# Performance work log

Hardware: AMD Instinct MI355X
Metric: run time of the kernel (lower is better)

The kernel has to match this reference:

```python
import jax, jax.numpy as jnp
import numpy as np

N, P, C = 100000, 48, 8
D, H = 64, 4
DH = D // H
FLAG = 7
EPS = 1e-5


def _layer_norm(x, g, b):
    mu = x.mean(-1, keepdims=True)
    var = ((x - mu) ** 2).mean(-1, keepdims=True)
    return (x - mu) * jax.lax.rsqrt(var + EPS) * g + b


def setup_inputs() -> dict:
    key = jax.random.key(0)
    ks = jax.random.split(key, 24)
    w = lambda k, shp: (jax.random.normal(k, shp, dtype=jnp.float32) * 0.05)
    inp = {
        "voxel_features": jax.random.normal(ks[0], (N, D), dtype=jnp.float32),
        "voxels": jax.random.normal(ks[1], (N, P, C), dtype=jnp.float32),
        "pp_w1": w(ks[2], (D, C)), "pp_b1": w(ks[3], (D,)),
        "pp_w2": w(ks[4], (D, D)), "pp_b2": w(ks[5], (D,)),
        "in_proj_w": w(ks[6], (3 * D, D)), "in_proj_b": w(ks[7], (3 * D,)),
        "out_w": w(ks[8], (D, D)), "out_b": w(ks[9], (D,)),
        "ln1_g": jnp.ones((D,), jnp.float32), "ln1_b": jnp.zeros((D,), jnp.float32),
        "ffn_w1": w(ks[10], (2 * D, D)), "ffn_b1": w(ks[11], (2 * D,)),
        "ffn_w2": w(ks[12], (D, 2 * D)), "ffn_b2": w(ks[13], (D,)),
        "ln2_g": jnp.ones((D,), jnp.float32), "ln2_b": jnp.zeros((D,), jnp.float32),
        "op_w1": w(ks[14], (D, D)), "op_b1": w(ks[15], (D,)),
        "op_w2": w(ks[16], (D, D)), "op_b2": w(ks[17], (D,)),
        "num_points": jax.random.randint(ks[18], (N,), 0, P, dtype=jnp.int32),
    }
    return inp


def reference(voxel_features, voxels, pp_w1, pp_b1, pp_w2, pp_b2,
              in_proj_w, in_proj_b, out_w, out_b, ln1_g, ln1_b,
              ffn_w1, ffn_b1, ffn_w2, ffn_b2, ln2_g, ln2_b,
              op_w1, op_b1, op_w2, op_b2, num_points):
    n, p, _ = voxels.shape
    point_mask = jnp.arange(p)[None, :] < num_points[:, None]          # [N,P]
    current_mask = (voxels[:, :, FLAG] > 0.5) & point_mask             # [N,P]
    history_mask = point_mask & ~current_mask                          # [N,P]
    history_present = history_mask.any(axis=1, keepdims=True)          # [N,1]

    point_features = voxels[:, :, :C]

    def masked_mean(vals, mask):
        m = mask.astype(vals.dtype)[..., None]
        counts = jnp.clip(mask.sum(1, keepdims=True), 1, None).astype(vals.dtype)
        return (vals * m).sum(1) / counts                              # [N,C]

    cur_sum = masked_mean(point_features, current_mask)
    his_sum = masked_mean(point_features, history_mask)

    def point_proj(x):
        return jax.nn.relu(x @ pp_w1.T + pp_b1) @ pp_w2.T + pp_b2

    tokens = jnp.stack([voxel_features, point_proj(cur_sum), point_proj(his_sum)], axis=1)  # [N,3,D]

    key_pad = jnp.stack([jnp.zeros((n,), bool),
                         ~current_mask.any(1),
                         ~history_present[:, 0]], axis=1)              # [N,3]

    # multi-head self-attention over 3 tokens
    qkv = tokens @ in_proj_w.T + in_proj_b                             # [N,3,3D]
    q, k, v = jnp.split(qkv, 3, axis=-1)
    q = q.reshape(n, 3, H, DH).transpose(0, 2, 1, 3)                   # [N,H,3,DH]
    k = k.reshape(n, 3, H, DH).transpose(0, 2, 1, 3)
    v = v.reshape(n, 3, H, DH).transpose(0, 2, 1, 3)
    scores = jnp.einsum('nhqd,nhkd->nhqk', q, k) / np.sqrt(DH)
    scores = jnp.where(key_pad[:, None, None, :], -jnp.inf, scores)
    attn = jax.nn.softmax(scores, axis=-1)
    ctx = jnp.einsum('nhqk,nhkd->nhqd', attn, v)                       # [N,H,3,DH]
    ctx = ctx.transpose(0, 2, 1, 3).reshape(n, 3, D)
    attn_out = ctx @ out_w.T + out_b

    tokens = _layer_norm(tokens + attn_out, ln1_g, ln1_b)
    ffn = jax.nn.relu(tokens @ ffn_w1.T + ffn_b1) @ ffn_w2.T + ffn_b2
    tokens = _layer_norm(tokens + ffn, ln2_g, ln2_b)

    refined = jax.nn.relu(tokens[:, 0] @ op_w1.T + op_b1) @ op_w2.T + op_b2
    refined = refined * history_present.astype(refined.dtype)
    return voxel_features + refined
```

## Files before the change

kernel.cpp:

```cpp
#include <hip/hip_runtime.h>


using bf16x8 = __attribute__((ext_vector_type(8))) __bf16;
using f32x4  = __attribute__((ext_vector_type(4))) float;

#define DEV static __device__ __forceinline__

DEV float bf2f(unsigned short u){
  union { unsigned int i; float f; } v; v.i = ((unsigned int)u) << 16; return v.f;
}
DEV unsigned short f2bf(float f){
  union { float f; unsigned int i; } v; v.f = f;
  unsigned int x = v.i;
  x += 0x7FFFu + ((x >> 16) & 1u);
  return (unsigned short)(x >> 16);
}

DEV unsigned short* lp(unsigned short* base, int row, int col){
  int byte = (col << 1) ^ ((row & 7) << 4);
  return (unsigned short*)((char*)base + (row << 7) + byte);
}

DEV bf16x8 ldA(const unsigned short* base, int mt, int kt, int lane){
  int row = mt*16 + (lane & 15);
  int col = kt*32 + ((lane >> 4) << 3);
  return *(const bf16x8*)lp((unsigned short*)base, row, col);
}
DEV bf16x8 ldB(const unsigned short* w, int frag, int lane){
  return *(const bf16x8*)(w + (size_t)frag*512 + (size_t)lane*8);
}
DEV void stC(unsigned short* base, int mt, int nt, f32x4 c, int lane){
  int col  = nt*16 + (lane & 15);
  int row0 = mt*16 + ((lane >> 4) << 2);
  #pragma unroll
  for (int r = 0; r < 4; ++r) *lp(base, row0 + r, col) = f2bf(c[r]);
}
DEV f32x4 MF(bf16x8 a, bf16x8 b, f32x4 c){
  return __builtin_amdgcn_mfma_f32_16x16x32_bf16(a, b, c, 0, 0, 0);
}

DEV void ld16(const unsigned short* base, int row, int col0, float* o){
  uint4 a = *(const uint4*)lp((unsigned short*)base, row, col0);
  uint4 b = *(const uint4*)lp((unsigned short*)base, row, col0 + 8);
  unsigned int w[8] = {a.x, a.y, a.z, a.w, b.x, b.y, b.z, b.w};
  #pragma unroll
  for (int i = 0; i < 8; ++i){
    union { unsigned int u; float f; } lo, hi;
    lo.u = w[i] << 16; hi.u = w[i] & 0xFFFF0000u;
    o[2*i] = lo.f; o[2*i+1] = hi.f;
  }
}
DEV void st16(unsigned short* base, int row, int col0, const float* f){
  unsigned int w[8];
  #pragma unroll
  for (int i = 0; i < 8; ++i)
    w[i] = (unsigned int)f2bf(f[2*i]) | ((unsigned int)f2bf(f[2*i+1]) << 16);
  *(uint4*)lp(base, row, col0)     = make_uint4(w[0], w[1], w[2], w[3]);
  *(uint4*)lp(base, row, col0 + 8) = make_uint4(w[4], w[5], w[6], w[7]);
}

DEV bf16x8 pack8(const float* f){
  union { bf16x8 v; unsigned short u[8]; } r;
  #pragma unroll
  for (int i = 0; i < 8; ++i) r.u[i] = f2bf(f[i]);
  return r.v;
}

DEV void layer_norm16(f32x4 x[4], const float* g, const float* b, int lane){
  float s[4], s2[4];
  #pragma unroll
  for (int r = 0; r < 4; ++r){
    s[r]  = x[0][r] + x[1][r] + x[2][r] + x[3][r];
    s2[r] = x[0][r]*x[0][r] + x[1][r]*x[1][r] + x[2][r]*x[2][r] + x[3][r]*x[3][r];
  }
  #pragma unroll
  for (int o = 1; o <= 8; o <<= 1){
    #pragma unroll
    for (int r = 0; r < 4; ++r){
      s[r]  += __shfl_xor(s[r],  o);
      s2[r] += __shfl_xor(s2[r], o);
    }
  }
  float mu[4], rs[4];
  #pragma unroll
  for (int r = 0; r < 4; ++r){
    mu[r] = s[r] * (1.f/64.f);
    float var = s2[r] * (1.f/64.f) - mu[r]*mu[r];
    rs[r] = rsqrtf(var + 1e-5f);
  }
  const int cl = lane & 15;
  #pragma unroll
  for (int nt = 0; nt < 4; ++nt){
    float gg = g[nt*16 + cl], bb = b[nt*16 + cl];
    #pragma unroll
    for (int r = 0; r < 4; ++r)
      x[nt][r] = (x[nt][r] - mu[r]) * rs[r] * gg + bb;
  }
}

__global__ void tva_pack_weights(const float* __restrict__ pp_w1, const float* __restrict__ pp_w2,
                                 const float* __restrict__ in_proj_w, const float* __restrict__ out_w,
                                 const float* __restrict__ ffn_w1, const float* __restrict__ ffn_w2,
                                 const float* __restrict__ op_w1, const float* __restrict__ op_w2,
                                 unsigned short* __restrict__ ws)
{
  int b = blockIdx.x, lane = threadIdx.x;
  const float* W; int base, ktiles, K;
  if      (b < 4)  { W = pp_w1;     base = 0;  ktiles = 1; K = 8;   }
  else if (b < 12) { W = pp_w2;     base = 4;  ktiles = 2; K = 64;  }
  else if (b < 36) { W = in_proj_w; base = 12; ktiles = 2; K = 64;  }
  else if (b < 44) { W = out_w;     base = 36; ktiles = 2; K = 64;  }
  else if (b < 60) { W = ffn_w1;    base = 44; ktiles = 2; K = 64;  }
  else if (b < 76) { W = ffn_w2;    base = 60; ktiles = 4; K = 128; }
  else if (b < 84) { W = op_w1;     base = 76; ktiles = 2; K = 64;  }
  else             { W = op_w2;     base = 84; ktiles = 2; K = 64;  }
  int local = b - base;
  int nt = local / ktiles, kt = local % ktiles;
  int n  = nt*16 + (lane & 15);
  int k0 = kt*32 + ((lane >> 4) << 3);
  unsigned short* dst = ws + (size_t)b*512 + (size_t)lane*8;
  #pragma unroll
  for (int i = 0; i < 8; ++i){
    int k = k0 + i;
    float v = (k < K) ? W[(size_t)n*K + k] : 0.0f;
    dst[i] = f2bf(v);
  }
}

__global__ __launch_bounds__(256)
void tva_main(const float* __restrict__ vf, const float* __restrict__ vox,
              const int* __restrict__ num_points,
              const float* __restrict__ pp_b1, const float* __restrict__ pp_b2,
              const float* __restrict__ ipb,  const float* __restrict__ outb,
              const float* __restrict__ ln1g, const float* __restrict__ ln1b,
              const float* __restrict__ f1b,  const float* __restrict__ f2bv,
              const float* __restrict__ ln2g, const float* __restrict__ ln2b,
              const float* __restrict__ o1b,  const float* __restrict__ o2b,
              const unsigned short* __restrict__ wfrag,
              float* __restrict__ out, int nvox)
{
  __shared__ unsigned short smem[4 * 64 * 64];
  const int tid  = threadIdx.x;
  const int wv   = tid >> 6;
  const int lane = tid & 63;
  unsigned short* X = smem + wv * (64*64);
  unsigned short* Q = X + 48*64;

  const int v0 = (blockIdx.x * 4 + wv) * 16;
  if (v0 >= nvox) return;
  const int cl = lane & 15;
  const int r0 = (lane >> 4) << 2;

  const int vi = lane >> 2, pq = lane & 3;
  const int np = num_points[v0 + vi];
  float cs[8] = {0,0,0,0,0,0,0,0}, hs[8] = {0,0,0,0,0,0,0,0};
  float cc = 0.f, hc = 0.f;
  const float4* vp = (const float4*)(vox + (size_t)(v0 + vi) * 384);
  #pragma unroll
  for (int k = 0; k < 12; ++k){
    int p = pq + (k << 2);
    float4 a = vp[p*2], b = vp[p*2 + 1];
    float pm = (p < np) ? 1.f : 0.f;
    float cm = (b.w > 0.5f) ? pm : 0.f;
    float hm = pm - cm;
    cc += cm; hc += hm;
    cs[0] += a.x*cm; cs[1] += a.y*cm; cs[2] += a.z*cm; cs[3] += a.w*cm;
    cs[4] += b.x*cm; cs[5] += b.y*cm; cs[6] += b.z*cm; cs[7] += b.w*cm;
    hs[0] += a.x*hm; hs[1] += a.y*hm; hs[2] += a.z*hm; hs[3] += a.w*hm;
    hs[4] += b.x*hm; hs[5] += b.y*hm; hs[6] += b.z*hm; hs[7] += b.w*hm;
  }
  #pragma unroll
  for (int o = 1; o <= 2; o <<= 1){
    cc += __shfl_xor(cc, o); hc += __shfl_xor(hc, o);
    #pragma unroll
    for (int j = 0; j < 8; ++j){
      cs[j] += __shfl_xor(cs[j], o);
      hs[j] += __shfl_xor(hs[j], o);
    }
  }
  const float icc = 1.f / fmaxf(cc, 1.f);
  const float ihc = 1.f / fmaxf(hc, 1.f);
  const unsigned int myfw = (cc > 0.f ? 1u : 0u) | (hc > 0.f ? 2u : 0u);

  bf16x8 ac, ah;
  {
    const int src = cl * 4;
    float cf[8], hf[8];
    #pragma unroll
    for (int i = 0; i < 8; ++i){
      cf[i] = __shfl(cs[i]*icc, src);
      hf[i] = __shfl(hs[i]*ihc, src);
    }
    union { bf16x8 v; unsigned short u[8]; } rc, rh;
    #pragma unroll
    for (int i = 0; i < 8; ++i){
      rc.u[i] = (lane < 16) ? f2bf(cf[i]) : (unsigned short)0;
      rh.u[i] = (lane < 16) ? f2bf(hf[i]) : (unsigned short)0;
    }
    ac = rc.v; ah = rh.v;
  }

  #pragma unroll
  for (int nt = 0; nt < 4; ++nt){
    float bb = pp_b1[nt*16 + cl];
    f32x4 c0 = {bb, bb, bb, bb}, c1 = {bb, bb, bb, bb};
    bf16x8 B = ldB(wfrag, nt, lane);
    c0 = MF(ac, B, c0);
    c1 = MF(ah, B, c1);
    #pragma unroll
    for (int r = 0; r < 4; ++r){ c0[r] = fmaxf(c0[r], 0.f); c1[r] = fmaxf(c1[r], 0.f); }
    stC(X, 0, nt, c0, lane);
    stC(X, 1, nt, c1, lane);
  }
  {
    bf16x8 hfr[2][2];
    #pragma unroll
    for (int m = 0; m < 2; ++m)
      #pragma unroll
      for (int kt = 0; kt < 2; ++kt) hfr[m][kt] = ldA(X, m, kt, lane);
    #pragma unroll
    for (int m = 0; m < 2; ++m){
      #pragma unroll
      for (int nt = 0; nt < 4; ++nt){
        float bb = pp_b2[nt*16 + cl];
        f32x4 c = {bb, bb, bb, bb};
        c = MF(hfr[m][0], ldB(wfrag, 4 + nt*2 + 0, lane), c);
        c = MF(hfr[m][1], ldB(wfrag, 4 + nt*2 + 1, lane), c);
        stC(X, m, nt, c, lane);
      }
    }
  }

  bf16x8 at[3][2];
  {
    const float* s = vf + (size_t)(v0 + cl) * 64 + ((lane >> 4) << 3);
    #pragma unroll
    for (int kt = 0; kt < 2; ++kt){
      float4 x0 = *(const float4*)(s + kt*32);
      float4 x1 = *(const float4*)(s + kt*32 + 4);
      float f[8] = {x0.x, x0.y, x0.z, x0.w, x1.x, x1.y, x1.z, x1.w};
      at[0][kt] = pack8(f);
    }
    #pragma unroll
    for (int kt = 0; kt < 2; ++kt){
      at[1][kt] = ldA(X, 0, kt, lane);
      at[2][kt] = ldA(X, 1, kt, lane);
    }
  }
  #pragma unroll
  for (int nt = 0; nt < 4; ++nt){
    float bb = ipb[nt*16 + cl];
    f32x4 c = {bb, bb, bb, bb};
    c = MF(at[0][0], ldB(wfrag, 12 + nt*2 + 0, lane), c);
    c = MF(at[0][1], ldB(wfrag, 12 + nt*2 + 1, lane), c);
    #pragma unroll
    for (int r = 0; r < 4; ++r) c[r] *= 0.25f;
    stC(Q, 0, nt, c, lane);
  }
  #pragma unroll
  for (int m = 0; m < 3; ++m){
    #pragma unroll
    for (int nt = 0; nt < 4; ++nt){
      int ntg = 4 + nt;
      float bb = ipb[64 + nt*16 + cl];
      f32x4 c = {bb, bb, bb, bb};
      c = MF(at[m][0], ldB(wfrag, 12 + ntg*2 + 0, lane), c);
      c = MF(at[m][1], ldB(wfrag, 12 + ntg*2 + 1, lane), c);
      stC(X, m, nt, c, lane);
    }
  }

  const int av = cl, hh2 = lane >> 4;
  float p0, p1, p2;
  {
    unsigned int fw = (unsigned int)__shfl((int)myfw, av*4);
    bool caZ = (fw & 1u) != 0, hpZ = (fw & 2u) != 0;
    float q[16]; ld16(Q, av, hh2*16, q);
    float sc[3];
    #pragma unroll
    for (int m = 0; m < 3; ++m){
      float kv[16]; ld16(X, m*16 + av, hh2*16, kv);
      float d = 0.f;
      #pragma unroll
      for (int j = 0; j < 16; ++j) d += q[j]*kv[j];
      sc[m] = d;
    }
    float mx = sc[0];
    mx = caZ ? fmaxf(mx, sc[1]) : mx;
    mx = hpZ ? fmaxf(mx, sc[2]) : mx;
    p0 = __expf(sc[0] - mx);
    p1 = caZ ? __expf(sc[1] - mx) : 0.f;
    p2 = hpZ ? __expf(sc[2] - mx) : 0.f;
    float inv = 1.f / (p0 + p1 + p2);
    p0 *= inv; p1 *= inv; p2 *= inv;
  }

  #pragma unroll
  for (int m = 0; m < 3; ++m){
    #pragma unroll
    for (int nt = 0; nt < 4; ++nt){
      int ntg = 8 + nt;
      float bb = ipb[128 + nt*16 + cl];
      f32x4 c = {bb, bb, bb, bb};
      c = MF(at[m][0], ldB(wfrag, 12 + ntg*2 + 0, lane), c);
      c = MF(at[m][1], ldB(wfrag, 12 + ntg*2 + 1, lane), c);
      stC(X, m, nt, c, lane);
    }
  }

  {
    float ctx[16];
    float vv[16];
    ld16(X, av, hh2*16, vv);
    #pragma unroll
    for (int j = 0; j < 16; ++j) ctx[j] = p0*vv[j];
    ld16(X, 16 + av, hh2*16, vv);
    #pragma unroll
    for (int j = 0; j < 16; ++j) ctx[j] += p1*vv[j];
    ld16(X, 32 + av, hh2*16, vv);
    #pragma unroll
    for (int j = 0; j < 16; ++j) ctx[j] += p2*vv[j];
    st16(Q, av, hh2*16, ctx);
  }

  f32x4 res1[4];
  {
    bf16x8 a0 = ldA(Q, 0, 0, lane), a1 = ldA(Q, 0, 1, lane);
    float rv[16];
    #pragma unroll
    for (int nt = 0; nt < 4; ++nt)
      #pragma unroll
      for (int r = 0; r < 4; ++r)
        rv[nt*4 + r] = vf[(size_t)(v0 + r0 + r)*64 + nt*16 + cl];
    #pragma unroll
    for (int nt = 0; nt < 4; ++nt){
      float bb = outb[nt*16 + cl];
      f32x4 c = {bb, bb, bb, bb};
      c = MF(a0, ldB(wfrag, 36 + nt*2 + 0, lane), c);
      c = MF(a1, ldB(wfrag, 36 + nt*2 + 1, lane), c);
      #pragma unroll
      for (int r = 0; r < 4; ++r) c[r] += rv[nt*4 + r];
      res1[nt] = c;
    }
    layer_norm16(res1, ln1g, ln1b, lane);
    #pragma unroll
    for (int nt = 0; nt < 4; ++nt) stC(Q, 0, nt, res1[nt], lane);
  }

  f32x4 tk2[4];
  {
    bf16x8 a0 = ldA(Q, 0, 0, lane), a1 = ldA(Q, 0, 1, lane);
    #pragma unroll
    for (int nt = 0; nt < 4; ++nt){
      float bb = f2bv[nt*16 + cl];
      tk2[nt] = (f32x4){bb, bb, bb, bb};
    }
    #pragma unroll
    for (int nt = 0; nt < 4; ++nt){
      float bb = f1b[nt*16 + cl];
      f32x4 c = {bb, bb, bb, bb};
      c = MF(a0, ldB(wfrag, 44 + nt*2 + 0, lane), c);
      c = MF(a1, ldB(wfrag, 44 + nt*2 + 1, lane), c);
      #pragma unroll
      for (int r = 0; r < 4; ++r) c[r] = fmaxf(c[r], 0.f);
      stC(X, 0, nt, c, lane);
    }
    {
      bf16x8 h0 = ldA(X, 0, 0, lane), h1 = ldA(X, 0, 1, lane);
      #pragma unroll
      for (int nt = 0; nt < 4; ++nt){
        tk2[nt] = MF(h0, ldB(wfrag, 60 + nt*4 + 0, lane), tk2[nt]);
        tk2[nt] = MF(h1, ldB(wfrag, 60 + nt*4 + 1, lane), tk2[nt]);
      }
    }
    #pragma unroll
    for (int nt = 4; nt < 8; ++nt){
      float bb = f1b[nt*16 + cl];
      f32x4 c = {bb, bb, bb, bb};
      c = MF(a0, ldB(wfrag, 44 + nt*2 + 0, lane), c);
      c = MF(a1, ldB(wfrag, 44 + nt*2 + 1, lane), c);
      #pragma unroll
      for (int r = 0; r < 4; ++r) c[r] = fmaxf(c[r], 0.f);
      stC(X, 0, nt - 4, c, lane);
    }
    {
      bf16x8 h0 = ldA(X, 0, 0, lane), h1 = ldA(X, 0, 1, lane);
      #pragma unroll
      for (int nt = 0; nt < 4; ++nt){
        tk2[nt] = MF(h0, ldB(wfrag, 60 + nt*4 + 2, lane), tk2[nt]);
        tk2[nt] = MF(h1, ldB(wfrag, 60 + nt*4 + 3, lane), tk2[nt]);
      }
    }
    #pragma unroll
    for (int nt = 0; nt < 4; ++nt)
      #pragma unroll
      for (int r = 0; r < 4; ++r) tk2[nt][r] += res1[nt][r];
    layer_norm16(tk2, ln2g, ln2b, lane);
    #pragma unroll
    for (int nt = 0; nt < 4; ++nt) stC(Q, 0, nt, tk2[nt], lane);
  }

  {
    bf16x8 a0 = ldA(Q, 0, 0, lane), a1 = ldA(Q, 0, 1, lane);
    #pragma unroll
    for (int nt = 0; nt < 4; ++nt){
      float bb = o1b[nt*16 + cl];
      f32x4 c = {bb, bb, bb, bb};
      c = MF(a0, ldB(wfrag, 76 + nt*2 + 0, lane), c);
      c = MF(a1, ldB(wfrag, 76 + nt*2 + 1, lane), c);
      #pragma unroll
      for (int r = 0; r < 4; ++r) c[r] = fmaxf(c[r], 0.f);
      stC(X, 0, nt, c, lane);
    }
    bf16x8 b0 = ldA(X, 0, 0, lane), b1 = ldA(X, 0, 1, lane);
    #pragma unroll
    for (int nt = 0; nt < 4; ++nt){
      float bb = o2b[nt*16 + cl];
      f32x4 c = {bb, bb, bb, bb};
      c = MF(b0, ldB(wfrag, 84 + nt*2 + 0, lane), c);
      c = MF(b1, ldB(wfrag, 84 + nt*2 + 1, lane), c);
      #pragma unroll
      for (int r = 0; r < 4; ++r){
        int row = r0 + r;
        unsigned int fw2 = (unsigned int)__shfl((int)myfw, row*4);
        float keep = (fw2 & 2u) ? 1.f : 0.f;
        size_t idx = (size_t)(v0 + row)*64 + nt*16 + cl;
        out[idx] = vf[idx] + keep * c[r];
      }
    }
  }
}

extern "C" void kernel_launch(void* const* d_in, const int* in_sizes, int n_in,
                              void* d_out, int out_size, void* d_ws, size_t ws_size,
                              hipStream_t stream)
{
  (void)n_in; (void)out_size; (void)ws_size;
  const float* vf    = (const float*)d_in[0];
  const float* vox   = (const float*)d_in[1];
  const float* pp_w1 = (const float*)d_in[2];
  const float* pp_b1 = (const float*)d_in[3];
  const float* pp_w2 = (const float*)d_in[4];
  const float* pp_b2 = (const float*)d_in[5];
  const float* ipw   = (const float*)d_in[6];
  const float* ipb   = (const float*)d_in[7];
  const float* outw  = (const float*)d_in[8];
  const float* outb  = (const float*)d_in[9];
  const float* ln1g  = (const float*)d_in[10];
  const float* ln1b  = (const float*)d_in[11];
  const float* f1w   = (const float*)d_in[12];
  const float* f1b   = (const float*)d_in[13];
  const float* f2w   = (const float*)d_in[14];
  const float* f2b   = (const float*)d_in[15];
  const float* ln2g  = (const float*)d_in[16];
  const float* ln2b  = (const float*)d_in[17];
  const float* o1w   = (const float*)d_in[18];
  const float* o1b   = (const float*)d_in[19];
  const float* o2w   = (const float*)d_in[20];
  const float* o2b   = (const float*)d_in[21];
  const int*   npts  = (const int*)d_in[22];
  unsigned short* wfrag = (unsigned short*)d_ws;
  float* out = (float*)d_out;

  const int nvox = in_sizes[0] / 64;
  const int ngrp = nvox / 16;
  const int nblk = (ngrp + 3) / 4;
  tva_pack_weights<<<92, 64, 0, stream>>>(pp_w1, pp_w2, ipw, outw, f1w, f2w, o1w, o2w, wfrag);
  tva_main<<<nblk, 256, 0, stream>>>(vf, vox, npts, pp_b1, pp_b2, ipb, outb,
                                     ln1g, ln1b, f1b, f2b, ln2g, ln2b, o1b, o2b,
                                     wfrag, out, nvox);
}
```

Baseline: 75.09 us.

## Swap MFMA operands so accumulators hold voxel-major rows, vectorising I/O and layernorm

Result: slower. 84.57 us (+12.6%).

```diff
diff --git a/kernel.cpp b/kernel.cpp
--- a/kernel.cpp
+++ b/kernel.cpp
@@ -6,9 +6,6 @@
 
 #define DEV static __device__ __forceinline__
 
-DEV float bf2f(unsigned short u){
-  union { unsigned int i; float f; } v; v.i = ((unsigned int)u) << 16; return v.f;
-}
 DEV unsigned short f2bf(float f){
   union { float f; unsigned int i; } v; v.f = f;
   unsigned int x = v.i;
@@ -21,22 +18,27 @@
   return (unsigned short*)((char*)base + (row << 7) + byte);
 }
 
-DEV bf16x8 ldA(const unsigned short* base, int mt, int kt, int lane){
-  int row = mt*16 + (lane & 15);
+DEV bf16x8 ldA(const unsigned short* base, int tt, int kt, int lane){
+  int row = tt*16 + (lane & 15);
   int col = kt*32 + ((lane >> 4) << 3);
   return *(const bf16x8*)lp((unsigned short*)base, row, col);
 }
-DEV bf16x8 ldB(const unsigned short* w, int frag, int lane){
+DEV bf16x8 ldW(const unsigned short* w, int frag, int lane){
   return *(const bf16x8*)(w + (size_t)frag*512 + (size_t)lane*8);
 }
-DEV void stC(unsigned short* base, int mt, int nt, f32x4 c, int lane){
-  int col  = nt*16 + (lane & 15);
-  int row0 = mt*16 + ((lane >> 4) << 2);
-  #pragma unroll
-  for (int r = 0; r < 4; ++r) *lp(base, row0 + r, col) = f2bf(c[r]);
+DEV void stC(unsigned short* base, int tt, int mt, f32x4 c, int lane){
+  int trow = tt*16 + (lane & 15);
+  int col0 = mt*16 + ((lane >> 4) << 2);
+  unsigned int lo = (unsigned int)f2bf(c[0]) | ((unsigned int)f2bf(c[1]) << 16);
+  unsigned int hi = (unsigned int)f2bf(c[2]) | ((unsigned int)f2bf(c[3]) << 16);
+  *(uint2*)lp(base, trow, col0) = make_uint2(lo, hi);
 }
 DEV f32x4 MF(bf16x8 a, bf16x8 b, f32x4 c){
   return __builtin_amdgcn_mfma_f32_16x16x32_bf16(a, b, c, 0, 0, 0);
+}
+DEV f32x4 bias4(const float* p){
+  float4 b = *(const float4*)p;
+  return (f32x4){b.x, b.y, b.z, b.w};
 }
 
 DEV void ld16(const unsigned short* base, int row, int col0, float* o){
@@ -66,35 +68,25 @@
   return r.v;
 }
 
-DEV void layer_norm16(f32x4 x[4], const float* g, const float* b, int lane){
-  float s[4], s2[4];
-  #pragma unroll
-  for (int r = 0; r < 4; ++r){
-    s[r]  = x[0][r] + x[1][r] + x[2][r] + x[3][r];
-    s2[r] = x[0][r]*x[0][r] + x[1][r]*x[1][r] + x[2][r]*x[2][r] + x[3][r]*x[3][r];
-  }
-  #pragma unroll
-  for (int o = 1; o <= 8; o <<= 1){
-    #pragma unroll
-    for (int r = 0; r < 4; ++r){
-      s[r]  += __shfl_xor(s[r],  o);
-      s2[r] += __shfl_xor(s2[r], o);
-    }
-  }
-  float mu[4], rs[4];
-  #pragma unroll
-  for (int r = 0; r < 4; ++r){
-    mu[r] = s[r] * (1.f/64.f);
-    float var = s2[r] * (1.f/64.f) - mu[r]*mu[r];
-    rs[r] = rsqrtf(var + 1e-5f);
-  }
-  const int cl = lane & 15;
+DEV void layer_norm_sw(f32x4 x[4], const float* g, const float* b, int lane){
+  float s = 0.f, s2 = 0.f;
+  #pragma unroll
+  for (int nt = 0; nt < 4; ++nt)
+    #pragma unroll
+    for (int r = 0; r < 4; ++r){ s += x[nt][r]; s2 += x[nt][r]*x[nt][r]; }
+  s  += __shfl_xor(s, 16);  s2 += __shfl_xor(s2, 16);
+  s  += __shfl_xor(s, 32);  s2 += __shfl_xor(s2, 32);
+  float mu = s * (1.f/64.f);
+  float rs = rsqrtf(s2 * (1.f/64.f) - mu*mu + 1e-5f);
+  const int r0 = (lane >> 4) << 2;
   #pragma unroll
   for (int nt = 0; nt < 4; ++nt){
-    float gg = g[nt*16 + cl], bb = b[nt*16 + cl];
-    #pragma unroll
-    for (int r = 0; r < 4; ++r)
-      x[nt][r] = (x[nt][r] - mu[r]) * rs[r] * gg + bb;
+    float4 gg = *(const float4*)&g[nt*16 + r0];
+    float4 bb = *(const float4*)&b[nt*16 + r0];
+    x[nt][0] = (x[nt][0] - mu) * rs * gg.x + bb.x;
+    x[nt][1] = (x[nt][1] - mu) * rs * gg.y + bb.y;
+    x[nt][2] = (x[nt][2] - mu) * rs * gg.z + bb.z;
+    x[nt][3] = (x[nt][3] - mu) * rs * gg.w + bb.w;
   }
 }
 
@@ -202,11 +194,10 @@
 
   #pragma unroll
   for (int nt = 0; nt < 4; ++nt){
-    float bb = pp_b1[nt*16 + cl];
-    f32x4 c0 = {bb, bb, bb, bb}, c1 = {bb, bb, bb, bb};
-    bf16x8 B = ldB(wfrag, nt, lane);
-    c0 = MF(ac, B, c0);
-    c1 = MF(ah, B, c1);
+    f32x4 binit = bias4(&pp_b1[nt*16 + r0]);
+    bf16x8 W = ldW(wfrag, nt, lane);
+    f32x4 c0 = MF(W, ac, binit);
+    f32x4 c1 = MF(W, ah, binit);
     #pragma unroll
     for (int r = 0; r < 4; ++r){ c0[r] = fmaxf(c0[r], 0.f); c1[r] = fmaxf(c1[r], 0.f); }
     stC(X, 0, nt, c0, lane);
@@ -219,13 +210,14 @@
       #pragma unroll
       for (int kt = 0; kt < 2; ++kt) hfr[m][kt] = ldA(X, m, kt, lane);
     #pragma unroll
-    for (int m = 0; m < 2; ++m){
-      #pragma unroll
-      for (int nt = 0; nt < 4; ++nt){
-        float bb = pp_b2[nt*16 + cl];
-        f32x4 c = {bb, bb, bb, bb};
-        c = MF(hfr[m][0], ldB(wfrag, 4 + nt*2 + 0, lane), c);
-        c = MF(hfr[m][1], ldB(wfrag, 4 + nt*2 + 1, lane), c);
+    for (int nt = 0; nt < 4; ++nt){
+      f32x4 binit = bias4(&pp_b2[nt*16 + r0]);
+      bf16x8 W0 = ldW(wfrag, 4 + nt*2 + 0, lane);
+      bf16x8 W1 = ldW(wfrag, 4 + nt*2 + 1, lane);
+      #pragma unroll
+      for (int m = 0; m < 2; ++m){
+        f32x4 c = MF(W0, hfr[m][0], binit);
+        c = MF(W1, hfr[m][1], c);
         stC(X, m, nt, c, lane);
       }
     }
@@ -249,23 +241,23 @@
   }
   #pragma unroll
   for (int nt = 0; nt < 4; ++nt){
-    float bb = ipb[nt*16 + cl];
-    f32x4 c = {bb, bb, bb, bb};
-    c = MF(at[0][0], ldB(wfrag, 12 + nt*2 + 0, lane), c);
-    c = MF(at[0][1], ldB(wfrag, 12 + nt*2 + 1, lane), c);
+    f32x4 c = bias4(&ipb[nt*16 + r0]);
+    c = MF(ldW(wfrag, 12 + nt*2 + 0, lane), at[0][0], c);
+    c = MF(ldW(wfrag, 12 + nt*2 + 1, lane), at[0][1], c);
     #pragma unroll
     for (int r = 0; r < 4; ++r) c[r] *= 0.25f;
     stC(Q, 0, nt, c, lane);
   }
   #pragma unroll
-  for (int m = 0; m < 3; ++m){
-    #pragma unroll
-    for (int nt = 0; nt < 4; ++nt){
-      int ntg = 4 + nt;
-      float bb = ipb[64 + nt*16 + cl];
-      f32x4 c = {bb, bb, bb, bb};
-      c = MF(at[m][0], ldB(wfrag, 12 + ntg*2 + 0, lane), c);
-      c = MF(at[m][1], ldB(wfrag, 12 + ntg*2 + 1, lane), c);
+  for (int nt = 0; nt < 4; ++nt){
+    int ntg = 4 + nt;
+    f32x4 binit = bias4(&ipb[64 + nt*16 + r0]);
+    bf16x8 W0 = ldW(wfrag, 12 + ntg*2 + 0, lane);
+    bf16x8 W1 = ldW(wfrag, 12 + ntg*2 + 1, lane);
+    #pragma unroll
+    for (int m = 0; m < 3; ++m){
+      f32x4 c = MF(W0, at[m][0], binit);
+      c = MF(W1, at[m][1], c);
       stC(X, m, nt, c, lane);
     }
   }
@@ -288,22 +280,23 @@
     float mx = sc[0];
     mx = caZ ? fmaxf(mx, sc[1]) : mx;
     mx = hpZ ? fmaxf(mx, sc[2]) : mx;
-    p0 = __expf(sc[0] - mx);
-    p1 = caZ ? __expf(sc[1] - mx) : 0.f;
-    p2 = hpZ ? __expf(sc[2] - mx) : 0.f;
-    float inv = 1.f / (p0 + p1 + p2);
-    p0 *= inv; p1 *= inv; p2 *= inv;
-  }
-
-  #pragma unroll
-  for (int m = 0; m < 3; ++m){
-    #pragma unroll
-    for (int nt = 0; nt < 4; ++nt){
-      int ntg = 8 + nt;
-      float bb = ipb[128 + nt*16 + cl];
-      f32x4 c = {bb, bb, bb, bb};
-      c = MF(at[m][0], ldB(wfrag, 12 + ntg*2 + 0, lane), c);
-      c = MF(at[m][1], ldB(wfrag, 12 + ntg*2 + 1, lane), c);
+    float e0 = __expf(sc[0] - mx);
+    float e1 = caZ ? __expf(sc[1] - mx) : 0.f;
+    float e2 = hpZ ? __expf(sc[2] - mx) : 0.f;
+    float inv = 1.f / (e0 + e1 + e2);
+    p0 = e0*inv; p1 = e1*inv; p2 = e2*inv;
+  }
+
+  #pragma unroll
+  for (int nt = 0; nt < 4; ++nt){
+    int ntg = 8 + nt;
+    f32x4 binit = bias4(&ipb[128 + nt*16 + r0]);
+    bf16x8 W0 = ldW(wfrag, 12 + ntg*2 + 0, lane);
+    bf16x8 W1 = ldW(wfrag, 12 + ntg*2 + 1, lane);
+    #pragma unroll
+    for (int m = 0; m < 3; ++m){
+      f32x4 c = MF(W0, at[m][0], binit);
+      c = MF(W1, at[m][1], c);
       stC(X, m, nt, c, lane);
     }
   }
@@ -326,23 +319,16 @@
   f32x4 res1[4];
   {
     bf16x8 a0 = ldA(Q, 0, 0, lane), a1 = ldA(Q, 0, 1, lane);
-    float rv[16];
-    #pragma unroll
-    for (int nt = 0; nt < 4; ++nt)
-      #pragma unroll
-      for (int r = 0; r < 4; ++r)
-        rv[nt*4 + r] = vf[(size_t)(v0 + r0 + r)*64 + nt*16 + cl];
     #pragma unroll
     for (int nt = 0; nt < 4; ++nt){
-      float bb = outb[nt*16 + cl];
-      f32x4 c = {bb, bb, bb, bb};
-      c = MF(a0, ldB(wfrag, 36 + nt*2 + 0, lane), c);
-      c = MF(a1, ldB(wfrag, 36 + nt*2 + 1, lane), c);
-      #pragma unroll
-      for (int r = 0; r < 4; ++r) c[r] += rv[nt*4 + r];
+      f32x4 c = bias4(&outb[nt*16 + r0]);
+      c = MF(ldW(wfrag, 36 + nt*2 + 0, lane), a0, c);
+      c = MF(ldW(wfrag, 36 + nt*2 + 1, lane), a1, c);
+      float4 rv = *(const float4*)&vf[(size_t)(v0 + cl)*64 + nt*16 + r0];
+      c[0] += rv.x; c[1] += rv.y; c[2] += rv.z; c[3] += rv.w;
       res1[nt] = c;
     }
-    layer_norm16(res1, ln1g, ln1b, lane);
+    layer_norm_sw(res1, ln1g, ln1b, lane);
     #pragma unroll
     for (int nt = 0; nt < 4; ++nt) stC(Q, 0, nt, res1[nt], lane);
   }
@@ -351,16 +337,12 @@
   {
     bf16x8 a0 = ldA(Q, 0, 0, lane), a1 = ldA(Q, 0, 1, lane);
     #pragma unroll
+    for (int nt = 0; nt < 4; ++nt) tk2[nt] = bias4(&f2bv[nt*16 + r0]);
+    #pragma unroll
     for (int nt = 0; nt < 4; ++nt){
-      float bb = f2bv[nt*16 + cl];
-      tk2[nt] = (f32x4){bb, bb, bb, bb};
-    }
-    #pragma unroll
-    for (int nt = 0; nt < 4; ++nt){
-      float bb = f1b[nt*16 + cl];
-      f32x4 c = {bb, bb, bb, bb};
-      c = MF(a0, ldB(wfrag, 44 + nt*2 + 0, lane), c);
-      c = MF(a1, ldB(wfrag, 44 + nt*2 + 1, lane), c);
+      f32x4 c = bias4(&f1b[nt*16 + r0]);
+      c = MF(ldW(wfrag, 44 + nt*2 + 0, lane), a0, c);
+      c = MF(ldW(wfrag, 44 + nt*2 + 1, lane), a1, c);
       #pragma unroll
       for (int r = 0; r < 4; ++r) c[r] = fmaxf(c[r], 0.f);
       stC(X, 0, nt, c, lane);
@@ -369,16 +351,15 @@
       bf16x8 h0 = ldA(X, 0, 0, lane), h1 = ldA(X, 0, 1, lane);
       #pragma unroll
       for (int nt = 0; nt < 4; ++nt){
-        tk2[nt] = MF(h0, ldB(wfrag, 60 + nt*4 + 0, lane), tk2[nt]);
-        tk2[nt] = MF(h1, ldB(wfrag, 60 + nt*4 + 1, lane), tk2[nt]);
+        tk2[nt] = MF(ldW(wfrag, 60 + nt*4 + 0, lane), h0, tk2[nt]);
+        tk2[nt] = MF(ldW(wfrag, 60 + nt*4 + 1, lane), h1, tk2[nt]);
       }
     }
     #pragma unroll
     for (int nt = 4; nt < 8; ++nt){
-      float bb = f1b[nt*16 + cl];
-      f32x4 c = {bb, bb, bb, bb};
-      c = MF(a0, ldB(wfrag, 44 + nt*2 + 0, lane), c);
-      c = MF(a1, ldB(wfrag, 44 + nt*2 + 1, lane), c);
+      f32x4 c = bias4(&f1b[nt*16 + r0]);
+      c = MF(ldW(wfrag, 44 + nt*2 + 0, lane), a0, c);
+      c = MF(ldW(wfrag, 44 + nt*2 + 1, lane), a1, c);
       #pragma unroll
       for (int r = 0; r < 4; ++r) c[r] = fmaxf(c[r], 0.f);
       stC(X, 0, nt - 4, c, lane);
@@ -387,15 +368,15 @@
       bf16x8 h0 = ldA(X, 0, 0, lane), h1 = ldA(X, 0, 1, lane);
       #pragma unroll
       for (int nt = 0; nt < 4; ++nt){
-        tk2[nt] = MF(h0, ldB(wfrag, 60 + nt*4 + 2, lane), tk2[nt]);
-        tk2[nt] = MF(h1, ldB(wfrag, 60 + nt*4 + 3, lane), tk2[nt]);
+        tk2[nt] = MF(ldW(wfrag, 60 + nt*4 + 2, lane), h0, tk2[nt]);
+        tk2[nt] = MF(ldW(wfrag, 60 + nt*4 + 3, lane), h1, tk2[nt]);
       }
     }
     #pragma unroll
     for (int nt = 0; nt < 4; ++nt)
       #pragma unroll
       for (int r = 0; r < 4; ++r) tk2[nt][r] += res1[nt][r];
-    layer_norm16(tk2, ln2g, ln2b, lane);
+    layer_norm_sw(tk2, ln2g, ln2b, lane);
     #pragma unroll
     for (int nt = 0; nt < 4; ++nt) stC(Q, 0, nt, tk2[nt], lane);
   }
@@ -404,29 +385,29 @@
     bf16x8 a0 = ldA(Q, 0, 0, lane), a1 = ldA(Q, 0, 1, lane);
     #pragma unroll
     for (int nt = 0; nt < 4; ++nt){
-      float bb = o1b[nt*16 + cl];
-      f32x4 c = {bb, bb, bb, bb};
-      c = MF(a0, ldB(wfrag, 76 + nt*2 + 0, lane), c);
-      c = MF(a1, ldB(wfrag, 76 + nt*2 + 1, lane), c);
+      f32x4 c = bias4(&o1b[nt*16 + r0]);
+      c = MF(ldW(wfrag, 76 + nt*2 + 0, lane), a0, c);
+      c = MF(ldW(wfrag, 76 + nt*2 + 1, lane), a1, c);
       #pragma unroll
       for (int r = 0; r < 4; ++r) c[r] = fmaxf(c[r], 0.f);
       stC(X, 0, nt, c, lane);
     }
     bf16x8 b0 = ldA(X, 0, 0, lane), b1 = ldA(X, 0, 1, lane);
+    unsigned int fw2 = (unsigned int)__shfl((int)myfw, cl*4);
+    float keep = (fw2 & 2u) ? 1.f : 0.f;
     #pragma unroll
     for (int nt = 0; nt < 4; ++nt){
-      float bb = o2b[nt*16 + cl];
-      f32x4 c = {bb, bb, bb, bb};
-      c = MF(b0, ldB(wfrag, 84 + nt*2 + 0, lane), c);
-      c = MF(b1, ldB(wfrag, 84 + nt*2 + 1, lane), c);
-      #pragma unroll
-      for (int r = 0; r < 4; ++r){
-        int row = r0 + r;
-        unsigned int fw2 = (unsigned int)__shfl((int)myfw, row*4);
-        float keep = (fw2 & 2u) ? 1.f : 0.f;
-        size_t idx = (size_t)(v0 + row)*64 + nt*16 + cl;
-        out[idx] = vf[idx] + keep * c[r];
-      }
+      f32x4 c = bias4(&o2b[nt*16 + r0]);
+      c = MF(ldW(wfrag, 84 + nt*2 + 0, lane), b0, c);
+      c = MF(ldW(wfrag, 84 + nt*2 + 1, lane), b1, c);
+      size_t idx = (size_t)(v0 + cl)*64 + nt*16 + r0;
+      float4 rv = *(const float4*)&vf[idx];
+      float4 o;
+      o.x = rv.x + keep * c[0];
+      o.y = rv.y + keep * c[1];
+      o.z = rv.z + keep * c[2];
+      o.w = rv.w + keep * c[3];
+      *(float4*)&out[idx] = o;
     }
   }
 }
```

## Split point aggregation into separate coalesced kernel writing bf16 means and flags

Applied to the files above, without the earlier changes.

Result: slower. 81.18 us (+8.1%).

```diff
diff --git a/kernel.cpp b/kernel.cpp
--- a/kernel.cpp
+++ b/kernel.cpp
@@ -6,9 +6,6 @@
 
 #define DEV static __device__ __forceinline__
 
-DEV float bf2f(unsigned short u){
-  union { unsigned int i; float f; } v; v.i = ((unsigned int)u) << 16; return v.f;
-}
 DEV unsigned short f2bf(float f){
   union { float f; unsigned int i; } v; v.f = f;
   unsigned int x = v.i;
@@ -128,8 +125,61 @@
 }
 
 __global__ __launch_bounds__(256)
-void tva_main(const float* __restrict__ vf, const float* __restrict__ vox,
-              const int* __restrict__ num_points,
+void tva_aggregate(const float* __restrict__ vox, const int* __restrict__ num_points,
+                   unsigned short* __restrict__ means, int* __restrict__ flags, int nvox)
+{
+  const int tid  = threadIdx.x;
+  const int wv   = tid >> 6, lane = tid & 63;
+  const int j    = lane & 7;
+  const int v    = (blockIdx.x*4 + wv)*8 + (lane >> 3);
+  if (v >= nvox) return;
+  const int np = num_points[v];
+  const float4* base = (const float4*)(vox + (size_t)v*384);
+  float s[4] = {0,0,0,0}, h[4] = {0,0,0,0};
+  float cc = 0.f, hc = 0.f;
+  #pragma unroll
+  for (int k = 0; k < 12; ++k){
+    float4 x = base[j + 8*k];
+    int p = 4*k + (j >> 1);
+    float fl = __shfl_xor(x.w, 1);
+    fl = (j & 1) ? x.w : fl;
+    float pm = (p < np) ? 1.f : 0.f;
+    float cm = (fl > 0.5f) ? pm : 0.f;
+    float hm = pm - cm;
+    cc += cm; hc += hm;
+    s[0] += x.x*cm; s[1] += x.y*cm; s[2] += x.z*cm; s[3] += x.w*cm;
+    h[0] += x.x*hm; h[1] += x.y*hm; h[2] += x.z*hm; h[3] += x.w*hm;
+  }
+  #pragma unroll
+  for (int o = 2; o <= 4; o <<= 1){
+    cc += __shfl_xor(cc, o); hc += __shfl_xor(hc, o);
+    #pragma unroll
+    for (int q = 0; q < 4; ++q){
+      s[q] += __shfl_xor(s[q], o);
+      h[q] += __shfl_xor(h[q], o);
+    }
+  }
+  const float icc = 1.f / fmaxf(cc, 1.f);
+  const float ihc = 1.f / fmaxf(hc, 1.f);
+  unsigned short* mp = means + (size_t)v*16;
+  if (j < 2){
+    ushort4 w;
+    w.x = f2bf(s[0]*icc); w.y = f2bf(s[1]*icc);
+    w.z = f2bf(s[2]*icc); w.w = f2bf(s[3]*icc);
+    *(ushort4*)(mp + j*4) = w;
+  } else if (j < 4){
+    ushort4 w;
+    w.x = f2bf(h[0]*ihc); w.y = f2bf(h[1]*ihc);
+    w.z = f2bf(h[2]*ihc); w.w = f2bf(h[3]*ihc);
+    *(ushort4*)(mp + 8 + (j-2)*4) = w;
+  } else if (j == 4){
+    flags[v] = (cc > 0.f ? 1 : 0) | (hc > 0.f ? 2 : 0);
+  }
+}
+
+__global__ __launch_bounds__(256)
+void tva_main(const float* __restrict__ vf,
+              const unsigned short* __restrict__ means, const int* __restrict__ flags,
               const float* __restrict__ pp_b1, const float* __restrict__ pp_b2,
               const float* __restrict__ ipb,  const float* __restrict__ outb,
               const float* __restrict__ ln1g, const float* __restrict__ ln1b,
@@ -151,53 +201,18 @@
   const int cl = lane & 15;
   const int r0 = (lane >> 4) << 2;
 
-  const int vi = lane >> 2, pq = lane & 3;
-  const int np = num_points[v0 + vi];
-  float cs[8] = {0,0,0,0,0,0,0,0}, hs[8] = {0,0,0,0,0,0,0,0};
-  float cc = 0.f, hc = 0.f;
-  const float4* vp = (const float4*)(vox + (size_t)(v0 + vi) * 384);
-  #pragma unroll
-  for (int k = 0; k < 12; ++k){
-    int p = pq + (k << 2);
-    float4 a = vp[p*2], b = vp[p*2 + 1];
-    float pm = (p < np) ? 1.f : 0.f;
-    float cm = (b.w > 0.5f) ? pm : 0.f;
-    float hm = pm - cm;
-    cc += cm; hc += hm;
-    cs[0] += a.x*cm; cs[1] += a.y*cm; cs[2] += a.z*cm; cs[3] += a.w*cm;
-    cs[4] += b.x*cm; cs[5] += b.y*cm; cs[6] += b.z*cm; cs[7] += b.w*cm;
-    hs[0] += a.x*hm; hs[1] += a.y*hm; hs[2] += a.z*hm; hs[3] += a.w*hm;
-    hs[4] += b.x*hm; hs[5] += b.y*hm; hs[6] += b.z*hm; hs[7] += b.w*hm;
-  }
-  #pragma unroll
-  for (int o = 1; o <= 2; o <<= 1){
-    cc += __shfl_xor(cc, o); hc += __shfl_xor(hc, o);
-    #pragma unroll
-    for (int j = 0; j < 8; ++j){
-      cs[j] += __shfl_xor(cs[j], o);
-      hs[j] += __shfl_xor(hs[j], o);
-    }
-  }
-  const float icc = 1.f / fmaxf(cc, 1.f);
-  const float ihc = 1.f / fmaxf(hc, 1.f);
-  const unsigned int myfw = (cc > 0.f ? 1u : 0u) | (hc > 0.f ? 2u : 0u);
-
+  const int fwv = flags[v0 + cl];
   bf16x8 ac, ah;
   {
-    const int src = cl * 4;
-    float cf[8], hf[8];
-    #pragma unroll
-    for (int i = 0; i < 8; ++i){
-      cf[i] = __shfl(cs[i]*icc, src);
-      hf[i] = __shfl(hs[i]*ihc, src);
-    }
-    union { bf16x8 v; unsigned short u[8]; } rc, rh;
-    #pragma unroll
-    for (int i = 0; i < 8; ++i){
-      rc.u[i] = (lane < 16) ? f2bf(cf[i]) : (unsigned short)0;
-      rh.u[i] = (lane < 16) ? f2bf(hf[i]) : (unsigned short)0;
-    }
-    ac = rc.v; ah = rh.v;
+    union { bf16x8 v; unsigned short u[8]; } z;
+    #pragma unroll
+    for (int i = 0; i < 8; ++i) z.u[i] = 0;
+    ac = z.v; ah = z.v;
+    if (lane < 16){
+      const unsigned short* mp = means + (size_t)(v0 + cl)*16;
+      ac = *(const bf16x8*)mp;
+      ah = *(const bf16x8*)(mp + 8);
+    }
   }
 
   #pragma unroll
@@ -273,8 +288,7 @@
   const int av = cl, hh2 = lane >> 4;
   float p0, p1, p2;
   {
-    unsigned int fw = (unsigned int)__shfl((int)myfw, av*4);
-    bool caZ = (fw & 1u) != 0, hpZ = (fw & 2u) != 0;
+    bool caZ = (fwv & 1) != 0, hpZ = (fwv & 2) != 0;
     float q[16]; ld16(Q, av, hh2*16, q);
     float sc[3];
     #pragma unroll
@@ -288,11 +302,11 @@
     float mx = sc[0];
     mx = caZ ? fmaxf(mx, sc[1]) : mx;
     mx = hpZ ? fmaxf(mx, sc[2]) : mx;
-    p0 = __expf(sc[0] - mx);
-    p1 = caZ ? __expf(sc[1] - mx) : 0.f;
-    p2 = hpZ ? __expf(sc[2] - mx) : 0.f;
-    float inv = 1.f / (p0 + p1 + p2);
-    p0 *= inv; p1 *= inv; p2 *= inv;
+    float e0 = __expf(sc[0] - mx);
+    float e1 = caZ ? __expf(sc[1] - mx) : 0.f;
+    float e2 = hpZ ? __expf(sc[2] - mx) : 0.f;
+    float inv = 1.f / (e0 + e1 + e2);
+    p0 = e0*inv; p1 = e1*inv; p2 = e2*inv;
   }
 
   #pragma unroll
@@ -422,8 +436,8 @@
       #pragma unroll
       for (int r = 0; r < 4; ++r){
         int row = r0 + r;
-        unsigned int fw2 = (unsigned int)__shfl((int)myfw, row*4);
-        float keep = (fw2 & 2u) ? 1.f : 0.f;
+        int fwr = flags[v0 + row];
+        float keep = (fwr & 2) ? 1.f : 0.f;
         size_t idx = (size_t)(v0 + row)*64 + nt*16 + cl;
         out[idx] = vf[idx] + keep * c[r];
       }
@@ -459,14 +473,20 @@
   const float* o2w   = (const float*)d_in[20];
   const float* o2b   = (const float*)d_in[21];
   const int*   npts  = (const int*)d_in[22];
+  float* out = (float*)d_out;
+
+  const int nvox = in_sizes[0] / 64;
   unsigned short* wfrag = (unsigned short*)d_ws;
-  float* out = (float*)d_out;
-
-  const int nvox = in_sizes[0] / 64;
-  const int ngrp = nvox / 16;
-  const int nblk = (ngrp + 3) / 4;
+  unsigned short* means = (unsigned short*)((char*)d_ws + 94208);
+  int*            flags = (int*)((char*)d_ws + 94208 + (size_t)nvox*32);
+
+  const int nblkA = (nvox + 31) / 32;
+  const int ngrp  = (nvox + 15) / 16;
+  const int nblkB = (ngrp + 3) / 4;
+
   tva_pack_weights<<<92, 64, 0, stream>>>(pp_w1, pp_w2, ipw, outw, f1w, f2w, o1w, o2w, wfrag);
-  tva_main<<<nblk, 256, 0, stream>>>(vf, vox, npts, pp_b1, pp_b2, ipb, outb,
-                                     ln1g, ln1b, f1b, f2b, ln2g, ln2b, o1b, o2b,
-                                     wfrag, out, nvox);
-}
+  tva_aggregate<<<nblkA, 256, 0, stream>>>(vox, npts, means, flags, nvox);
+  tva_main<<<nblkB, 256, 0, stream>>>(vf, means, flags, pp_b1, pp_b2, ipb, outb,
+                                      ln1g, ln1b, f1b, f2b, ln2g, ln2b, o1b, o2b,
+                                      wfrag, out, nvox);
+}
```
